# Optimization experiments

Measured on AMD Instinct MI355X. Metric: run time of the kernel, lower is better.

Reference implementation:

```python
import jax, jax.numpy as jnp
import numpy as np

QMAX = 127.0

def quantize_int8(x):
    # symmetric per-row (per-token) int8 quantization
    scale = jnp.max(jnp.abs(x), axis=-1, keepdims=True) / QMAX  # [N,1]
    scale = jnp.maximum(scale, 1e-8)
    q = jnp.clip(jnp.round(x / scale), -QMAX, QMAX).astype(jnp.int8)
    return q, scale


def setup_inputs() -> dict:
    key = jax.random.key(0)
    k1, k2 = jax.random.split(key)
    in_features, out_features = 4096, 4096
    x = jax.random.normal(k1, (4, 2048, in_features), dtype=jnp.float32)
    # weight buffer: randint(1, 128) int8, shape (out, in)
    weight = jax.random.randint(k2, (out_features, in_features), 1, 128, dtype=jnp.int32).astype(jnp.int8)
    weight_scale = jnp.ones((1,), dtype=jnp.float32)
    return {"x": x, "weight": weight, "weight_scale": weight_scale}


def reference(x, weight, weight_scale):
    x_shape = x.shape
    xf = x.reshape(-1, x_shape[-1])  # [N, in]
    q, scale_x = quantize_int8(xf)
    acc = jnp.matmul(q, weight.T, preferred_element_type=jnp.int32)  # [N, out]
    y = acc.astype(jnp.float32) * scale_x * weight_scale[0]
    return y.reshape(*x_shape[:-1], -1)
```

## Files before the change

kernel.cpp:

```cpp
#include <hip/hip_runtime.h>
#include <cstdint>

typedef int v4i __attribute__((ext_vector_type(4)));

#define K_DIM 4096
#define BM 256
#define BN 256
#define BK 64
#define NT (K_DIM / BK)
#define TILE_BYTES (BM * BK)
#define BUF_STRIDE (2 * TILE_BYTES)

__global__ __launch_bounds__(256) void pack_weight(
    const int* __restrict__ w32, int8_t* __restrict__ w8, int total16)
{
    const int i = blockIdx.x * 256 + threadIdx.x;
    if (i >= total16) return;
    const v4i* src = reinterpret_cast<const v4i*>(w32) + i * 4;
    v4i out;
#pragma unroll
    for (int j = 0; j < 4; ++j) {
        const v4i v = src[j];
        out[j] = (v.x & 0xff) | ((v.y & 0xff) << 8) |
                 ((v.z & 0xff) << 16) | ((unsigned)(v.w & 0xff) << 24);
    }
    reinterpret_cast<v4i*>(w8)[i] = out;
}

__global__ __launch_bounds__(256) void quant_rows(
    const float* __restrict__ x, int8_t* __restrict__ q,
    float* __restrict__ scales)
{
    const int row = blockIdx.x;
    const int t   = threadIdx.x;
    const float4* xr4 = reinterpret_cast<const float4*>(x + (size_t)row * K_DIM);

    float4 v[4];
    float m = 0.0f;
#pragma unroll
    for (int i = 0; i < 4; ++i) {
        v[i] = xr4[i * 256 + t];
        m = fmaxf(m, fmaxf(fmaxf(fabsf(v[i].x), fabsf(v[i].y)),
                           fmaxf(fabsf(v[i].z), fabsf(v[i].w))));
    }
#pragma unroll
    for (int off = 32; off >= 1; off >>= 1)
        m = fmaxf(m, __shfl_xor(m, off, 64));

    __shared__ float wmax[4];
    if ((t & 63) == 0) wmax[t >> 6] = m;
    __syncthreads();
    const float am = fmaxf(fmaxf(wmax[0], wmax[1]), fmaxf(wmax[2], wmax[3]));
    const float s  = fmaxf(am / 127.0f, 1e-8f);
    if (t == 0) scales[row] = s;

    int* qi = reinterpret_cast<int*>(q + (size_t)row * K_DIM);
#pragma unroll
    for (int i = 0; i < 4; ++i) {
        const float e[4] = {v[i].x, v[i].y, v[i].z, v[i].w};
        unsigned packed = 0;
#pragma unroll
        for (int j = 0; j < 4; ++j) {
            float r = rintf(e[j] / s);
            r = fminf(fmaxf(r, -127.0f), 127.0f);
            packed |= ((unsigned)((int)r & 0xff)) << (8 * j);
        }
        qi[i * 256 + t] = (int)packed;
    }
}

__global__ __launch_bounds__(512, 2) void gemm_i8(
    const int8_t* __restrict__ A,
    const int8_t* __restrict__ B,
    const float* __restrict__ sA,
    const float* __restrict__ wsc,
    float* __restrict__ C,
    int M, int N)
{
    __shared__ int8_t lds[3 * BUF_STRIDE];

    const int t    = threadIdx.x;
    const int lane = t & 63;
    const int w    = t >> 6;
    const int wr   = w >> 2;
    const int wc   = w & 3;

    const int nwg = gridDim.x;
    int bid = blockIdx.x;
    if ((nwg & 7) == 0) bid = (bid & 7) * (nwg >> 3) + (bid >> 3);
    const int ntn  = N / BN;
    const int brow = (bid / ntn) * BM;
    const int bcol = (bid % ntn) * BN;

    const int idx0 = t;
    const int idx1 = t + 512;
    const int r0 = idx0 >> 2, r1 = idx1 >> 2;
    const int c0 = (((idx0 & 3) ^ ((r0 >> 1) & 3)) << 4);
    const int c1 = (((idx1 & 3) ^ ((r1 >> 1) & 3)) << 4);
    const int8_t* gA0 = A + (size_t)(brow + r0) * K_DIM + c0;
    const int8_t* gA1 = A + (size_t)(brow + r1) * K_DIM + c1;
    const int8_t* gB0 = B + (size_t)(bcol + r0) * K_DIM + c0;
    const int8_t* gB1 = B + (size_t)(bcol + r1) * K_DIM + c1;
    const int dst0 = idx0 * 16, dst1 = idx1 * 16;

#define GLDS(gp, off) \
    __builtin_amdgcn_global_load_lds( \
        (const __attribute__((address_space(1))) void*)(gp), \
        (__attribute__((address_space(3))) void*)(lds + (off)), 16, 0, 0)
#define STAGE_A(buf, tt) do { \
    GLDS(gA0 + (size_t)(tt) * BK, (buf) * BUF_STRIDE + dst0); \
    GLDS(gA1 + (size_t)(tt) * BK, (buf) * BUF_STRIDE + dst1); } while (0)
#define STAGE_B(buf, tt) do { \
    GLDS(gB0 + (size_t)(tt) * BK, (buf) * BUF_STRIDE + TILE_BYTES + dst0); \
    GLDS(gB1 + (size_t)(tt) * BK, (buf) * BUF_STRIDE + TILE_BYTES + dst1); } while (0)

    const int c16 = lane >> 4;
    int offA[2][4], offB[4];
#pragma unroll
    for (int mh = 0; mh < 2; ++mh)
#pragma unroll
        for (int m = 0; m < 4; ++m) {
            const int row = wr * 128 + mh * 64 + m * 16 + (lane & 15);
            offA[mh][m] = row * BK + ((c16 ^ ((row >> 1) & 3)) << 4);
        }
#pragma unroll
    for (int n = 0; n < 4; ++n) {
        const int row = wc * 64 + n * 16 + (lane & 15);
        offB[n] = TILE_BYTES + row * BK + ((c16 ^ ((row >> 1) & 3)) << 4);
    }

    v4i acc[8][4];
#pragma unroll
    for (int m = 0; m < 8; ++m)
#pragma unroll
        for (int n = 0; n < 4; ++n)
            acc[m][n] = (v4i){0, 0, 0, 0};

    STAGE_A(0, 0); STAGE_B(0, 0);
    STAGE_A(1, 1); STAGE_B(1, 1);
    asm volatile("s_waitcnt vmcnt(4)" ::: "memory");
    __builtin_amdgcn_s_barrier();

#define MFMA_Q(BASE) do { \
    acc[BASE+0][0] = __builtin_amdgcn_mfma_i32_16x16x64_i8(a0, b0, acc[BASE+0][0], 0,0,0); \
    acc[BASE+0][1] = __builtin_amdgcn_mfma_i32_16x16x64_i8(a0, b1, acc[BASE+0][1], 0,0,0); \
    acc[BASE+0][2] = __builtin_amdgcn_mfma_i32_16x16x64_i8(a0, b2, acc[BASE+0][2], 0,0,0); \
    acc[BASE+0][3] = __builtin_amdgcn_mfma_i32_16x16x64_i8(a0, b3, acc[BASE+0][3], 0,0,0); \
    acc[BASE+1][0] = __builtin_amdgcn_mfma_i32_16x16x64_i8(a1, b0, acc[BASE+1][0], 0,0,0); \
    acc[BASE+1][1] = __builtin_amdgcn_mfma_i32_16x16x64_i8(a1, b1, acc[BASE+1][1], 0,0,0); \
    acc[BASE+1][2] = __builtin_amdgcn_mfma_i32_16x16x64_i8(a1, b2, acc[BASE+1][2], 0,0,0); \
    acc[BASE+1][3] = __builtin_amdgcn_mfma_i32_16x16x64_i8(a1, b3, acc[BASE+1][3], 0,0,0); \
    acc[BASE+2][0] = __builtin_amdgcn_mfma_i32_16x16x64_i8(a2, b0, acc[BASE+2][0], 0,0,0); \
    acc[BASE+2][1] = __builtin_amdgcn_mfma_i32_16x16x64_i8(a2, b1, acc[BASE+2][1], 0,0,0); \
    acc[BASE+2][2] = __builtin_amdgcn_mfma_i32_16x16x64_i8(a2, b2, acc[BASE+2][2], 0,0,0); \
    acc[BASE+2][3] = __builtin_amdgcn_mfma_i32_16x16x64_i8(a2, b3, acc[BASE+2][3], 0,0,0); \
    acc[BASE+3][0] = __builtin_amdgcn_mfma_i32_16x16x64_i8(a3, b0, acc[BASE+3][0], 0,0,0); \
    acc[BASE+3][1] = __builtin_amdgcn_mfma_i32_16x16x64_i8(a3, b1, acc[BASE+3][1], 0,0,0); \
    acc[BASE+3][2] = __builtin_amdgcn_mfma_i32_16x16x64_i8(a3, b2, acc[BASE+3][2], 0,0,0); \
    acc[BASE+3][3] = __builtin_amdgcn_mfma_i32_16x16x64_i8(a3, b3, acc[BASE+3][3], 0,0,0); \
    } while (0)

    int cur = 0, nx = 2;
    for (int tt = 0; tt < NT; ++tt) {
        const int8_t* bufc = lds + cur * BUF_STRIDE;
        v4i a0, a1, a2, a3, b0, b1, b2, b3;
        a0 = *(const v4i*)(bufc + offA[0][0]);
        a1 = *(const v4i*)(bufc + offA[0][1]);
        a2 = *(const v4i*)(bufc + offA[0][2]);
        a3 = *(const v4i*)(bufc + offA[0][3]);
        b0 = *(const v4i*)(bufc + offB[0]);
        b1 = *(const v4i*)(bufc + offB[1]);
        b2 = *(const v4i*)(bufc + offB[2]);
        b3 = *(const v4i*)(bufc + offB[3]);
        if (tt + 2 < NT) STAGE_A(nx, tt + 2);
        __builtin_amdgcn_s_barrier();
        asm volatile("s_waitcnt lgkmcnt(0)" ::: "memory");
        __builtin_amdgcn_s_setprio(1);
        MFMA_Q(0);
        __builtin_amdgcn_s_setprio(0);
        __builtin_amdgcn_s_barrier();
        a0 = *(const v4i*)(bufc + offA[1][0]);
        a1 = *(const v4i*)(bufc + offA[1][1]);
        a2 = *(const v4i*)(bufc + offA[1][2]);
        a3 = *(const v4i*)(bufc + offA[1][3]);
        if (tt + 2 < NT) STAGE_B(nx, tt + 2);
        __builtin_amdgcn_s_barrier();
        asm volatile("s_waitcnt lgkmcnt(0)" ::: "memory");
        __builtin_amdgcn_s_setprio(1);
        MFMA_Q(4);
        __builtin_amdgcn_s_setprio(0);
        if (tt + 2 < NT)      asm volatile("s_waitcnt vmcnt(4)" ::: "memory");
        else if (tt + 1 < NT) asm volatile("s_waitcnt vmcnt(0)" ::: "memory");
        __builtin_amdgcn_s_barrier();
        cur = (cur == 2) ? 0 : cur + 1;
        nx  = (nx  == 2) ? 0 : nx  + 1;
    }

    const float wsv = wsc[0];
#pragma unroll
    for (int m = 0; m < 8; ++m) {
        const int rbase = brow + wr * 128 + m * 16 + (lane >> 4) * 4;
        float sc[4];
#pragma unroll
        for (int j = 0; j < 4; ++j) sc[j] = sA[rbase + j] * wsv;
#pragma unroll
        for (int n = 0; n < 4; ++n) {
            const int col = bcol + wc * 64 + n * 16 + (lane & 15);
#pragma unroll
            for (int j = 0; j < 4; ++j)
                C[(size_t)(rbase + j) * N + col] = (float)acc[m][n][j] * sc[j];
        }
    }
#undef GLDS
#undef STAGE_A
#undef STAGE_B
#undef MFMA_Q
}

extern "C" void kernel_launch(void* const* d_in, const int* in_sizes, int n_in,
                              void* d_out, int out_size, void* d_ws, size_t ws_size,
                              hipStream_t stream) {
    const float* x      = (const float*)d_in[0];
    const int*   w32    = (const int*)d_in[1];
    const float* wscale = (const float*)d_in[2];
    float*       out    = (float*)d_out;

    const int M = in_sizes[0] / K_DIM;
    const int N = in_sizes[1] / K_DIM;

    int8_t* q      = (int8_t*)d_ws;
    float*  scales = (float*)((char*)d_ws + (size_t)M * K_DIM);
    int8_t* w8     = (int8_t*)((char*)d_ws + (size_t)M * K_DIM + (size_t)M * sizeof(float));

    const int total16 = (N * K_DIM) / 16;
    pack_weight<<<(total16 + 255) / 256, 256, 0, stream>>>(w32, w8, total16);

    quant_rows<<<M, 256, 0, stream>>>(x, q, scales);

    const int nblk = (M / BM) * (N / BN);
    gemm_i8<<<nblk, 512, 0, stream>>>(q, w8, scales, wscale, out, M, N);
}
```

Before: 200.5 us.

## Deepen LDS pipeline to four stages with register-prefetched fragments and fewer barriers

Moves the int8 GEMM main loop from a 3-buffer to a 4-buffer LDS ring, issuing global→LDS loads three tiles ahead. The next tile's A and B fragments are prefetched into registers (ping-ponging the B registers across a 2x unrolled loop) while the current MFMAs run. LDS reads use inline ds_read_b128 with explicit lgkmcnt waits and sched_barriers, which cuts the per-tile workgroup barriers from three to one. The aim is to hide LDS and global latency behind MFMA work. The cost is more LDS per block (128KB) and more registers, plus correctness that now depends on hand-tuned wait counts.

```diff
diff --git a/kernel.cpp b/kernel.cpp
--- a/kernel.cpp
+++ b/kernel.cpp
@@ -10,6 +10,7 @@
 #define NT (K_DIM / BK)
 #define TILE_BYTES (BM * BK)
 #define BUF_STRIDE (2 * TILE_BYTES)
+#define NBUF 4
 
 __global__ __launch_bounds__(256) void pack_weight(
     const int* __restrict__ w32, int8_t* __restrict__ w8, int total16)
@@ -77,7 +78,7 @@
     float* __restrict__ C,
     int M, int N)
 {
-    __shared__ int8_t lds[3 * BUF_STRIDE];
+    __shared__ int8_t lds[NBUF * BUF_STRIDE];
 
     const int t    = threadIdx.x;
     const int lane = t & 63;
@@ -115,19 +116,22 @@
     GLDS(gB1 + (size_t)(tt) * BK, (buf) * BUF_STRIDE + TILE_BYTES + dst1); } while (0)
 
     const int c16 = lane >> 4;
-    int offA[2][4], offB[4];
-#pragma unroll
-    for (int mh = 0; mh < 2; ++mh)
-#pragma unroll
-        for (int m = 0; m < 4; ++m) {
-            const int row = wr * 128 + mh * 64 + m * 16 + (lane & 15);
-            offA[mh][m] = row * BK + ((c16 ^ ((row >> 1) & 3)) << 4);
-        }
+    unsigned offA0[4], offA1[4], offB[4];
+#pragma unroll
+    for (int m = 0; m < 4; ++m) {
+        int row0 = wr * 128 + m * 16 + (lane & 15);
+        int row1 = row0 + 64;
+        offA0[m] = row0 * BK + ((c16 ^ ((row0 >> 1) & 3)) << 4);
+        offA1[m] = row1 * BK + ((c16 ^ ((row1 >> 1) & 3)) << 4);
+    }
 #pragma unroll
     for (int n = 0; n < 4; ++n) {
-        const int row = wc * 64 + n * 16 + (lane & 15);
+        int row = wc * 64 + n * 16 + (lane & 15);
         offB[n] = TILE_BYTES + row * BK + ((c16 ^ ((row >> 1) & 3)) << 4);
     }
+
+#define DSREAD(dst, addr) \
+    asm volatile("ds_read_b128 %0, %1" : "=v"(dst) : "v"(addr))
 
     v4i acc[8][4];
 #pragma unroll
@@ -136,64 +140,82 @@
         for (int n = 0; n < 4; ++n)
             acc[m][n] = (v4i){0, 0, 0, 0};
 
+    v4i a0[4], a1[4], bA[4], bB[4];
+
     STAGE_A(0, 0); STAGE_B(0, 0);
     STAGE_A(1, 1); STAGE_B(1, 1);
+    STAGE_A(2, 2); STAGE_B(2, 2);
     asm volatile("s_waitcnt vmcnt(4)" ::: "memory");
     __builtin_amdgcn_s_barrier();
-
-#define MFMA_Q(BASE) do { \
-    acc[BASE+0][0] = __builtin_amdgcn_mfma_i32_16x16x64_i8(a0, b0, acc[BASE+0][0], 0,0,0); \
-    acc[BASE+0][1] = __builtin_amdgcn_mfma_i32_16x16x64_i8(a0, b1, acc[BASE+0][1], 0,0,0); \
-    acc[BASE+0][2] = __builtin_amdgcn_mfma_i32_16x16x64_i8(a0, b2, acc[BASE+0][2], 0,0,0); \
-    acc[BASE+0][3] = __builtin_amdgcn_mfma_i32_16x16x64_i8(a0, b3, acc[BASE+0][3], 0,0,0); \
-    acc[BASE+1][0] = __builtin_amdgcn_mfma_i32_16x16x64_i8(a1, b0, acc[BASE+1][0], 0,0,0); \
-    acc[BASE+1][1] = __builtin_amdgcn_mfma_i32_16x16x64_i8(a1, b1, acc[BASE+1][1], 0,0,0); \
-    acc[BASE+1][2] = __builtin_amdgcn_mfma_i32_16x16x64_i8(a1, b2, acc[BASE+1][2], 0,0,0); \
-    acc[BASE+1][3] = __builtin_amdgcn_mfma_i32_16x16x64_i8(a1, b3, acc[BASE+1][3], 0,0,0); \
-    acc[BASE+2][0] = __builtin_amdgcn_mfma_i32_16x16x64_i8(a2, b0, acc[BASE+2][0], 0,0,0); \
-    acc[BASE+2][1] = __builtin_amdgcn_mfma_i32_16x16x64_i8(a2, b1, acc[BASE+2][1], 0,0,0); \
-    acc[BASE+2][2] = __builtin_amdgcn_mfma_i32_16x16x64_i8(a2, b2, acc[BASE+2][2], 0,0,0); \
-    acc[BASE+2][3] = __builtin_amdgcn_mfma_i32_16x16x64_i8(a2, b3, acc[BASE+2][3], 0,0,0); \
-    acc[BASE+3][0] = __builtin_amdgcn_mfma_i32_16x16x64_i8(a3, b0, acc[BASE+3][0], 0,0,0); \
-    acc[BASE+3][1] = __builtin_amdgcn_mfma_i32_16x16x64_i8(a3, b1, acc[BASE+3][1], 0,0,0); \
-    acc[BASE+3][2] = __builtin_amdgcn_mfma_i32_16x16x64_i8(a3, b2, acc[BASE+3][2], 0,0,0); \
-    acc[BASE+3][3] = __builtin_amdgcn_mfma_i32_16x16x64_i8(a3, b3, acc[BASE+3][3], 0,0,0); \
+    __builtin_amdgcn_sched_barrier(0);
+
+    DSREAD(a0[0], offA0[0]); DSREAD(a0[1], offA0[1]);
+    DSREAD(a0[2], offA0[2]); DSREAD(a0[3], offA0[3]);
+    DSREAD(bA[0], offB[0]);  DSREAD(bA[1], offB[1]);
+    DSREAD(bA[2], offB[2]);  DSREAD(bA[3], offB[3]);
+
+#define MFMA_Q(BASE, AV, BV) do { \
+    acc[BASE+0][0] = __builtin_amdgcn_mfma_i32_16x16x64_i8(AV[0], BV[0], acc[BASE+0][0], 0,0,0); \
+    acc[BASE+0][1] = __builtin_amdgcn_mfma_i32_16x16x64_i8(AV[0], BV[1], acc[BASE+0][1], 0,0,0); \
+    acc[BASE+0][2] = __builtin_amdgcn_mfma_i32_16x16x64_i8(AV[0], BV[2], acc[BASE+0][2], 0,0,0); \
+    acc[BASE+0][3] = __builtin_amdgcn_mfma_i32_16x16x64_i8(AV[0], BV[3], acc[BASE+0][3], 0,0,0); \
+    acc[BASE+1][0] = __builtin_amdgcn_mfma_i32_16x16x64_i8(AV[1], BV[0], acc[BASE+1][0], 0,0,0); \
+    acc[BASE+1][1] = __builtin_amdgcn_mfma_i32_16x16x64_i8(AV[1], BV[1], acc[BASE+1][1], 0,0,0); \
+    acc[BASE+1][2] = __builtin_amdgcn_mfma_i32_16x16x64_i8(AV[1], BV[2], acc[BASE+1][2], 0,0,0); \
+    acc[BASE+1][3] = __builtin_amdgcn_mfma_i32_16x16x64_i8(AV[1], BV[3], acc[BASE+1][3], 0,0,0); \
+    acc[BASE+2][0] = __builtin_amdgcn_mfma_i32_16x16x64_i8(AV[2], BV[0], acc[BASE+2][0], 0,0,0); \
+    acc[BASE+2][1] = __builtin_amdgcn_mfma_i32_16x16x64_i8(AV[2], BV[1], acc[BASE+2][1], 0,0,0); \
+    acc[BASE+2][2] = __builtin_amdgcn_mfma_i32_16x16x64_i8(AV[2], BV[2], acc[BASE+2][2], 0,0,0); \
+    acc[BASE+2][3] = __builtin_amdgcn_mfma_i32_16x16x64_i8(AV[2], BV[3], acc[BASE+2][3], 0,0,0); \
+    acc[BASE+3][0] = __builtin_amdgcn_mfma_i32_16x16x64_i8(AV[3], BV[0], acc[BASE+3][0], 0,0,0); \
+    acc[BASE+3][1] = __builtin_amdgcn_mfma_i32_16x16x64_i8(AV[3], BV[1], acc[BASE+3][1], 0,0,0); \
+    acc[BASE+3][2] = __builtin_amdgcn_mfma_i32_16x16x64_i8(AV[3], BV[2], acc[BASE+3][2], 0,0,0); \
+    acc[BASE+3][3] = __builtin_amdgcn_mfma_i32_16x16x64_i8(AV[3], BV[3], acc[BASE+3][3], 0,0,0); \
     } while (0)
 
-    int cur = 0, nx = 2;
-    for (int tt = 0; tt < NT; ++tt) {
-        const int8_t* bufc = lds + cur * BUF_STRIDE;
-        v4i a0, a1, a2, a3, b0, b1, b2, b3;
-        a0 = *(const v4i*)(bufc + offA[0][0]);
-        a1 = *(const v4i*)(bufc + offA[0][1]);
-        a2 = *(const v4i*)(bufc + offA[0][2]);
-        a3 = *(const v4i*)(bufc + offA[0][3]);
-        b0 = *(const v4i*)(bufc + offB[0]);
-        b1 = *(const v4i*)(bufc + offB[1]);
-        b2 = *(const v4i*)(bufc + offB[2]);
-        b3 = *(const v4i*)(bufc + offB[3]);
-        if (tt + 2 < NT) STAGE_A(nx, tt + 2);
-        __builtin_amdgcn_s_barrier();
-        asm volatile("s_waitcnt lgkmcnt(0)" ::: "memory");
-        __builtin_amdgcn_s_setprio(1);
-        MFMA_Q(0);
-        __builtin_amdgcn_s_setprio(0);
-        __builtin_amdgcn_s_barrier();
-        a0 = *(const v4i*)(bufc + offA[1][0]);
-        a1 = *(const v4i*)(bufc + offA[1][1]);
-        a2 = *(const v4i*)(bufc + offA[1][2]);
-        a3 = *(const v4i*)(bufc + offA[1][3]);
-        if (tt + 2 < NT) STAGE_B(nx, tt + 2);
-        __builtin_amdgcn_s_barrier();
-        asm volatile("s_waitcnt lgkmcnt(0)" ::: "memory");
-        __builtin_amdgcn_s_setprio(1);
-        MFMA_Q(4);
-        __builtin_amdgcn_s_setprio(0);
-        if (tt + 2 < NT)      asm volatile("s_waitcnt vmcnt(4)" ::: "memory");
-        else if (tt + 1 < NT) asm volatile("s_waitcnt vmcnt(0)" ::: "memory");
-        __builtin_amdgcn_s_barrier();
-        cur = (cur == 2) ? 0 : cur + 1;
-        nx  = (nx  == 2) ? 0 : nx  + 1;
+#define TILE_BODY(T, BU, BL) do { \
+    const unsigned bufc = (unsigned)(cur * BUF_STRIDE); \
+    const unsigned bufn = (unsigned)(((cur + 1) & 3) * BUF_STRIDE); \
+    const int nx3 = (cur + 3) & 3; \
+     \
+    DSREAD(a1[0], bufc + offA1[0]); DSREAD(a1[1], bufc + offA1[1]); \
+    DSREAD(a1[2], bufc + offA1[2]); DSREAD(a1[3], bufc + offA1[3]); \
+    if ((T) + 3 < NT) STAGE_A(nx3, (T) + 3); \
+    asm volatile("s_waitcnt lgkmcnt(4)" ::: "memory"); \
+    __builtin_amdgcn_sched_barrier(0); \
+    __builtin_amdgcn_s_setprio(1); \
+    MFMA_Q(0, a0, BU); \
+    __builtin_amdgcn_s_setprio(0); \
+    __builtin_amdgcn_sched_barrier(0); \
+     \
+    if ((T) + 1 < NT) { \
+        DSREAD(a0[0], bufn + offA0[0]); DSREAD(a0[1], bufn + offA0[1]); \
+        DSREAD(a0[2], bufn + offA0[2]); DSREAD(a0[3], bufn + offA0[3]); \
+        DSREAD(BL[0], bufn + offB[0]);  DSREAD(BL[1], bufn + offB[1]); \
+        DSREAD(BL[2], bufn + offB[2]);  DSREAD(BL[3], bufn + offB[3]); \
+    } \
+    if ((T) + 3 < NT) STAGE_B(nx3, (T) + 3); \
+    if ((T) + 1 < NT) asm volatile("s_waitcnt lgkmcnt(8)" ::: "memory"); \
+    else              asm volatile("s_waitcnt lgkmcnt(0)" ::: "memory"); \
+    __builtin_amdgcn_sched_barrier(0); \
+    __builtin_amdgcn_s_setprio(1); \
+    MFMA_Q(4, a1, BU); \
+    __builtin_amdgcn_s_setprio(0); \
+    __builtin_amdgcn_sched_barrier(0); \
+     \
+    if ((T) + 1 < NT) { \
+        if ((T) + 3 < NT) asm volatile("s_waitcnt vmcnt(4)" ::: "memory"); \
+        else              asm volatile("s_waitcnt vmcnt(0)" ::: "memory"); \
+        __builtin_amdgcn_s_barrier(); \
+        __builtin_amdgcn_sched_barrier(0); \
+    } \
+    cur = (cur + 1) & 3; \
+    } while (0)
+
+    int cur = 0;
+    for (int tt = 0; tt < NT; tt += 2) {
+        TILE_BODY(tt,     bA, bB);
+        TILE_BODY(tt + 1, bB, bA);
     }
 
     const float wsv = wsc[0];
@@ -214,7 +236,9 @@
 #undef GLDS
 #undef STAGE_A
 #undef STAGE_B
+#undef DSREAD
 #undef MFMA_Q
+#undef TILE_BODY
 }
 
 extern "C" void kernel_launch(void* const* d_in, const int* in_sizes, int n_in,
```

Measured after the change: 196.5 us. 1.02x faster.
